# Optimization experiments

Hardware: AMD Instinct MI355X
Metric: run time of the kernel (lower is better)

## Reference

```python
import jax, jax.numpy as jnp
import numpy as np

N_NODES = 50000
N_EDGES = 320000
IN_FEAT = 128
HIDDEN = 256
N_CLASSES = 40
BN_EPS = 1e-5


def _gcn_norm(edge_index, n_nodes):
    # Add self-loops (PyG gcn_norm default) and compute sym-normalized weights
    loops = jnp.arange(n_nodes, dtype=edge_index.dtype)
    src = jnp.concatenate([edge_index[0], loops])
    dst = jnp.concatenate([edge_index[1], loops])
    ones = jnp.ones(src.shape[0], dtype=jnp.float32)
    deg = jax.ops.segment_sum(ones, dst, num_segments=n_nodes)
    dinv = jnp.where(deg > 0, jax.lax.rsqrt(deg), 0.0)
    norm = dinv[src] * dinv[dst]  # [E+N]
    return src, dst, norm


def _gcn_conv(x, src, dst, norm, W, b, n_nodes):
    xw = x @ W                                   # [N, F_out]
    msg = norm[:, None] * xw[src]                # [E+N, F_out] gather
    out = jax.ops.segment_sum(msg, dst, num_segments=n_nodes)  # scatter-add
    return out + b


def _batchnorm(x, gamma, beta):
    mean = jnp.mean(x, axis=0)
    var = jnp.mean(jnp.square(x - mean), axis=0)  # biased, training-mode stats
    return (x - mean) * jax.lax.rsqrt(var + BN_EPS) * gamma + beta


def setup_inputs() -> dict:
    key = jax.random.key(0)
    ks = jax.random.split(key, 8)
    x = jax.random.normal(ks[0], (N_NODES, IN_FEAT), dtype=jnp.float32)
    edge_index = jax.random.randint(ks[1], (2, N_EDGES), 0, N_NODES, dtype=jnp.int64)
    s1 = 1.0 / np.sqrt(IN_FEAT)
    s2 = 1.0 / np.sqrt(HIDDEN)
    return {
        "x": x,
        "edge_index": edge_index,
        "W1": jax.random.normal(ks[2], (IN_FEAT, HIDDEN), dtype=jnp.float32) * s1,
        "b1": jnp.zeros((HIDDEN,), dtype=jnp.float32),
        "g1": jnp.ones((HIDDEN,), dtype=jnp.float32),
        "be1": jnp.zeros((HIDDEN,), dtype=jnp.float32),
        "W2": jax.random.normal(ks[3], (HIDDEN, HIDDEN), dtype=jnp.float32) * s2,
        "b2": jnp.zeros((HIDDEN,), dtype=jnp.float32),
        "g2": jnp.ones((HIDDEN,), dtype=jnp.float32),
        "be2": jnp.zeros((HIDDEN,), dtype=jnp.float32),
        "W3": jax.random.normal(ks[4], (HIDDEN, N_CLASSES), dtype=jnp.float32) * s2,
        "b3": jnp.zeros((N_CLASSES,), dtype=jnp.float32),
    }


def reference(x, edge_index, W1, b1, g1, be1, W2, b2, g2, be2, W3, b3):
    n = x.shape[0]
    src, dst, norm = _gcn_norm(edge_index, n)
    # layer 1
    h = _gcn_conv(x, src, dst, norm, W1, b1, n)
    h = jax.nn.relu(_batchnorm(h, g1, be1))
    # layer 2
    h = _gcn_conv(h, src, dst, norm, W2, b2, n)
    h = jax.nn.relu(_batchnorm(h, g2, be2))
    # output layer
    h = _gcn_conv(h, src, dst, norm, W3, b3, n)
    return jax.nn.log_softmax(h, axis=1)
```

## Files before the change

### kernel.cpp

```cpp
#include <hip/hip_runtime.h>

#define N_NODES 50000
#define N_EDGES 320000
#define IN_FEAT 128
#define HIDDEN  256
#define NCLS    40
#define BN_EPS  1e-5f

#define SCAN_B  256
#define SCAN_NB ((N_NODES + SCAN_B - 1) / SCAN_B)
#define GNB     (N_NODES / 16)

#define PREP_HIST_NB  (N_EDGES / 256)
#define PREP_CVT_NB   (N_NODES * IN_FEAT / 8 / 256)
#define PREP_PACK_NB  54
#define BNA_NB        (N_NODES * HIDDEN / 8 / 256)

typedef __attribute__((ext_vector_type(8))) _Float16 f16x8;
typedef __attribute__((ext_vector_type(2))) _Float16 f16x2;
typedef __attribute__((ext_vector_type(4))) float f32x4;

__device__ __forceinline__ f16x2 pkmax0(f16x2 a) {
    return __builtin_elementwise_max(a, (f16x2)(_Float16)0.f);
}

__device__ __forceinline__ void packB_unit(const float* __restrict__ W,
                                           _Float16* __restrict__ Bp,
                                           int nt, int kt, int nkt, int M, int lane) {
    const int n = nt * 16 + (lane & 15);
    const int kb = kt * 32 + (lane >> 4) * 8;
    _Float16* dst = Bp + (((size_t)nt * nkt + kt) * 64 + lane) * 8;
#pragma unroll
    for (int j = 0; j < 8; j++)
        dst[j] = (n < M) ? (_Float16)W[(size_t)(kb + j) * M + n] : (_Float16)0.f;
}

__global__ __launch_bounds__(256) void k_prep(const int* __restrict__ e_dst,
                                              int* __restrict__ counts,
                                              const float* __restrict__ x,
                                              _Float16* __restrict__ Xh,
                                              const float* __restrict__ W1,
                                              const float* __restrict__ W2,
                                              const float* __restrict__ W3,
                                              _Float16* __restrict__ W1p,
                                              _Float16* __restrict__ W2p,
                                              _Float16* __restrict__ W3p) {
    const int b = blockIdx.x;
    const int tid = threadIdx.x;
    if (b < PREP_HIST_NB) {
        const int e = b * 256 + tid;
        atomicAdd(&counts[e_dst[e]], 1);
    } else if (b < PREP_HIST_NB + PREP_CVT_NB) {
        const int i = (b - PREP_HIST_NB) * 256 + tid;
        float4 a = *(const float4*)(x + (size_t)i * 8);
        float4 c = *(const float4*)(x + (size_t)i * 8 + 4);
        f16x8 o = {(_Float16)a.x, (_Float16)a.y, (_Float16)a.z, (_Float16)a.w,
                   (_Float16)c.x, (_Float16)c.y, (_Float16)c.z, (_Float16)c.w};
        *(f16x8*)&Xh[(size_t)i * 8] = o;
    } else {
        const int wave = tid >> 6, lane = tid & 63;
        const int u = (b - PREP_HIST_NB - PREP_CVT_NB) * 4 + wave;
        if (u < 64) {
            packB_unit(W1, W1p, u >> 2, u & 3, 4, HIDDEN, lane);
        } else if (u < 192) {
            const int v = u - 64;
            packB_unit(W2, W2p, v >> 3, v & 7, 8, HIDDEN, lane);
        } else {
            const int v = u - 192;
            packB_unit(W3, W3p, v >> 3, v & 7, 8, NCLS, lane);
        }
    }
}

__global__ __launch_bounds__(SCAN_B) void k_scan_local(const int* __restrict__ counts,
                                                       int* __restrict__ rowp,
                                                       int* __restrict__ partials) {
    __shared__ int s[SCAN_B];
    const int tid = threadIdx.x;
    const int i = blockIdx.x * SCAN_B + tid;
    int v = (i < N_NODES) ? counts[i] : 0;
    s[tid] = v;
    __syncthreads();
    for (int off = 1; off < SCAN_B; off <<= 1) {
        int t = (tid >= off) ? s[tid - off] : 0;
        __syncthreads();
        s[tid] += t;
        __syncthreads();
    }
    if (i < N_NODES) rowp[i] = s[tid] - v;
    if (tid == SCAN_B - 1) partials[blockIdx.x] = s[SCAN_B - 1];
}

__global__ __launch_bounds__(SCAN_B) void k_scan_add(int* __restrict__ rowp,
                                                     int* __restrict__ cursor,
                                                     const int* __restrict__ partials,
                                                     const int* __restrict__ counts,
                                                     float* __restrict__ dinv) {
    __shared__ int s[SCAN_B];
    const int tid = threadIdx.x;
    const int b = blockIdx.x;
    int v = (tid < b) ? partials[tid] : 0;
    s[tid] = v;
    __syncthreads();
    for (int off = SCAN_B / 2; off > 0; off >>= 1) {
        if (tid < off) s[tid] += s[tid + off];
        __syncthreads();
    }
    const int offset = s[0];
    const int i = b * SCAN_B + tid;
    if (i < N_NODES) {
        int r = rowp[i] + offset;
        rowp[i] = r;
        cursor[i] = r;
        dinv[i] = rsqrtf(1.0f + (float)counts[i]);
    }
    if (b == 0 && tid == 0) rowp[N_NODES] = N_EDGES;
}

__global__ void k_scatter(const int* __restrict__ src, const int* __restrict__ dst,
                          int* __restrict__ cursor, const float* __restrict__ dinv,
                          int2* __restrict__ edat) {
    int e = blockIdx.x * blockDim.x + threadIdx.x;
    if (e < N_EDGES) {
        int d = dst[e], s = src[e];
        int p = atomicAdd(&cursor[d], 1);
        int2 v; v.x = s; v.y = __float_as_int(dinv[s] * dinv[d]);
        edat[p] = v;
    }
}

template <int KIN>
__global__ __launch_bounds__(256, 4) void k_fused(const _Float16* __restrict__ Xin,
                                                  const int* __restrict__ rowp,
                                                  const int2* __restrict__ edat,
                                                  const float* __restrict__ dinv,
                                                  const _Float16* __restrict__ Bp,
                                                  const float* __restrict__ bias,
                                                  _Float16* __restrict__ C,
                                                  float* __restrict__ bnp2) {
    constexpr int nkt = KIN / 32;
    constexpr int LROW = KIN + 8;
    constexpr int RW8 = KIN / 8;
    constexpr int NL = KIN / 128;
    __shared__ __align__(16) _Float16 At[16 * LROW];
    const int wave = threadIdx.x >> 6;
    const int lane = threadIdx.x & 63;
    const int sub  = lane >> 4;
    const int t    = lane & 15;
    const int sb   = lane & 48;
    const int node = blockIdx.x * 16 + wave * 4 + sub;

    const int e0 = rowp[node];
    const int deg = rowp[node + 1] - e0;
    int   pidx = 0;
    float pw   = 0.f;
    if (t < deg) {
        const int2 e = edat[e0 + t];
        pidx = e.x;
        pw = __int_as_float(e.y);
    }
    const float dd = dinv[node];
    const f16x2 sw2 = (f16x2)(_Float16)(dd * dd);

    const f16x8* __restrict__ Xr = (const f16x8*)Xin;
    union U8 { f16x8 v; f16x2 h[4]; };

    U8 a[NL];
#pragma unroll
    for (int q = 0; q < NL; q++) {
        U8 r; r.v = Xr[(size_t)node * RW8 + q * 16 + t];
#pragma unroll
        for (int p = 0; p < 4; p++) a[q].h[p] = sw2 * r.h[p];
    }

    auto batch8 = [&](int j0) {
        int bi[8]; _Float16 bw[8];
#pragma unroll
        for (int j = 0; j < 8; j++) {
            const int   v  = __shfl(pidx, sb + j0 + j);
            const float wv = __shfl(pw,  sb + j0 + j);
            const bool ok = (j0 + j) < deg;
            bi[j] = ok ? v : node;
            bw[j] = ok ? (_Float16)wv : (_Float16)0.f;
        }
        U8 r[8][NL];
#pragma unroll
        for (int j = 0; j < 8; j++)
#pragma unroll
            for (int q = 0; q < NL; q++)
                r[j][q].v = Xr[(size_t)bi[j] * RW8 + q * 16 + t];
        __builtin_amdgcn_sched_barrier(0);
#pragma unroll
        for (int j = 0; j < 8; j++) {
            const f16x2 w2 = (f16x2)bw[j];
#pragma unroll
            for (int q = 0; q < NL; q++)
#pragma unroll
                for (int p = 0; p < 4; p++) a[q].h[p] = w2 * r[j][q].h[p] + a[q].h[p];
        }
    };
    batch8(0);
    if (__any(deg > 8)) {
        batch8(8);
        if (__any(deg > 16)) {
            for (int j = 16; j < deg; j++) {
                const int2 ed = edat[e0 + j];
                const f16x2 w2 = (f16x2)(_Float16)__int_as_float(ed.y);
#pragma unroll
                for (int q = 0; q < NL; q++) {
                    U8 r; r.v = Xr[(size_t)ed.x * RW8 + q * 16 + t];
#pragma unroll
                    for (int p = 0; p < 4; p++) a[q].h[p] = w2 * r.h[p] + a[q].h[p];
                }
            }
        }
    }
#pragma unroll
    for (int q = 0; q < NL; q++)
        *(f16x8*)&At[(wave * 4 + sub) * LROW + q * 128 + t * 8] = a[q].v;
    __syncthreads();

    const int rowb = blockIdx.x * 16;
    const int ntile0 = wave * 4;
    const _Float16* aL = &At[(lane & 15) * LROW + (lane >> 4) * 8];
    f32x4 acc[4] = {};
#pragma unroll
    for (int kt = 0; kt < nkt; kt++) {
        f16x8 af = *(const f16x8*)(aL + kt * 32);
#pragma unroll
        for (int nt = 0; nt < 4; nt++) {
            f16x8 bfr = *(const f16x8*)(Bp + (((size_t)(ntile0 + nt) * nkt + kt) * 64 + lane) * 8);
            acc[nt] = __builtin_amdgcn_mfma_f32_16x16x32_f16(af, bfr, acc[nt], 0, 0, 0);
        }
    }
    const int rg = lane >> 4, cc = lane & 15;
    float s[4], q2[4];
#pragma unroll
    for (int nt = 0; nt < 4; nt++) {
        const int col = (ntile0 + nt) * 16 + cc;
        const float b = bias[col];
        f32x4 a2 = acc[nt];
        a2[0] += b; a2[1] += b; a2[2] += b; a2[3] += b;
        const size_t base = (size_t)(rowb + rg * 4) * HIDDEN + col;
#pragma unroll
        for (int i = 0; i < 4; i++) C[base + (size_t)i * HIDDEN] = (_Float16)a2[i];
        s[nt] = a2[0] + a2[1] + a2[2] + a2[3];
        q2[nt] = a2[0]*a2[0] + a2[1]*a2[1] + a2[2]*a2[2] + a2[3]*a2[3];
    }
#pragma unroll
    for (int nt = 0; nt < 4; nt++) {
        s[nt] += __shfl_xor(s[nt], 16); s[nt] += __shfl_xor(s[nt], 32);
        q2[nt] += __shfl_xor(q2[nt], 16); q2[nt] += __shfl_xor(q2[nt], 32);
    }
    if (lane < 16) {
        float* dst = bnp2 + ((blockIdx.x & 31) * 512) + ntile0 * 16 + lane;
#pragma unroll
        for (int nt = 0; nt < 4; nt++) {
            atomicAdd(&dst[nt * 16], s[nt]);
            atomicAdd(&dst[nt * 16 + 256], q2[nt]);
        }
    }
}

__global__ __launch_bounds__(256) void k_bnprep(const float* __restrict__ bnp2,
                                                const float* __restrict__ g,
                                                const float* __restrict__ be,
                                                float* __restrict__ scale,
                                                float* __restrict__ shift) {
    const int f = threadIdx.x;
    float s = 0.f, q = 0.f;
#pragma unroll
    for (int b = 0; b < 32; b++) {
        s += bnp2[(size_t)b * 512 + f];
        q += bnp2[(size_t)b * 512 + 256 + f];
    }
    const float inv_n = 1.0f / (float)N_NODES;
    float mean = s * inv_n;
    float var = q * inv_n - mean * mean;
    var = fmaxf(var, 0.f);
    float sc = g[f] * rsqrtf(var + BN_EPS);
    scale[f] = sc;
    shift[f] = be[f] - mean * sc;
}

__global__ __launch_bounds__(256) void k_bnapply(_Float16* __restrict__ H,
                                                 const float* __restrict__ scale,
                                                 const float* __restrict__ shift) {
    const size_t i = (size_t)blockIdx.x * 256 + threadIdx.x;
    const int f0 = (int)(i & 31) * 8;
    union U8 { f16x8 v; f16x2 h[4]; } r;
    r.v = ((const f16x8*)H)[i];
#pragma unroll
    for (int p = 0; p < 4; p++) {
        f16x2 sc = {(_Float16)scale[f0 + 2 * p], (_Float16)scale[f0 + 2 * p + 1]};
        f16x2 sh = {(_Float16)shift[f0 + 2 * p], (_Float16)shift[f0 + 2 * p + 1]};
        r.h[p] = pkmax0(sc * r.h[p] + sh);
    }
    ((f16x8*)H)[i] = r.v;
}

template <int K_>
__global__ __launch_bounds__(64) void k_gemm3(const _Float16* __restrict__ A,
                                              const _Float16* __restrict__ Bp,
                                              const float* __restrict__ scale,
                                              const float* __restrict__ shift,
                                              _Float16* __restrict__ C) {
    constexpr int nkt = K_ / 32;
    constexpr int MT = 3;
    const int lane = threadIdx.x & 63;
    const int rowb = blockIdx.x * 16;
    const int koff = (lane >> 4) * 8;
    const _Float16* aptr = A + (size_t)(rowb + (lane & 15)) * K_ + koff;
    f32x4 acc[MT] = {};
#pragma unroll
    for (int kt = 0; kt < nkt; kt++) {
        union { f16x8 v; f16x2 h[4]; } au, tu;
        au.v = *(const f16x8*)(aptr + kt * 32);
        const int kb = kt * 32 + koff;
#pragma unroll
        for (int p = 0; p < 4; p++) {
            f16x2 sc2 = {(_Float16)scale[kb + 2 * p], (_Float16)scale[kb + 2 * p + 1]};
            f16x2 sh2 = {(_Float16)shift[kb + 2 * p], (_Float16)shift[kb + 2 * p + 1]};
            tu.h[p] = pkmax0(sc2 * au.h[p] + sh2);
        }
#pragma unroll
        for (int nt = 0; nt < MT; nt++) {
            f16x8 bfr = *(const f16x8*)(Bp + (((size_t)nt * nkt + kt) * 64 + lane) * 8);
            acc[nt] = __builtin_amdgcn_mfma_f32_16x16x32_f16(tu.v, bfr, acc[nt], 0, 0, 0);
        }
    }
    const int rg = lane >> 4, cc = lane & 15;
#pragma unroll
    for (int nt = 0; nt < MT; nt++) {
        const int col = nt * 16 + cc;
        if (col < NCLS) {
            const size_t base = (size_t)(rowb + rg * 4) * NCLS + col;
#pragma unroll
            for (int i = 0; i < 4; i++) C[base + (size_t)i * NCLS] = (_Float16)acc[nt][i];
        }
    }
}

__global__ __launch_bounds__(256) void k_out(const _Float16* __restrict__ XW,
                                             const int* __restrict__ rowp,
                                             const int2* __restrict__ edat,
                                             const float* __restrict__ dinv,
                                             const float* __restrict__ bias,
                                             float* __restrict__ out) {
    const int wave = threadIdx.x >> 6;
    const int lane = threadIdx.x & 63;
    const int node = blockIdx.x * 4 + wave;
    const float dd = dinv[node];
    const bool act = lane < NCLS;
    const int e0 = rowp[node];
    const int deg = rowp[node + 1] - e0;
    int pidx = 0; float pw = 0.f;
    if (lane < deg) {
        const int2 e = edat[e0 + lane];
        pidx = e.x; pw = __int_as_float(e.y);
    }
    const _Float16* Xl = XW + lane;
    float acc = 0.f;
    if (act) acc = dd * dd * (float)Xl[(size_t)node * NCLS];
    auto batch8 = [&](int j0) {
        int bi[8]; float bw[8];
#pragma unroll
        for (int j = 0; j < 8; j++) {
            const int   v  = __shfl(pidx, j0 + j);
            const float wv = __shfl(pw,  j0 + j);
            const bool ok = (j0 + j) < deg;
            bi[j] = ok ? v : node;
            bw[j] = ok ? wv : 0.f;
        }
        if (act) {
            float rv[8];
#pragma unroll
            for (int j = 0; j < 8; j++) rv[j] = (float)Xl[(size_t)bi[j] * NCLS];
            __builtin_amdgcn_sched_barrier(0);
#pragma unroll
            for (int j = 0; j < 8; j++) acc += bw[j] * rv[j];
        }
    };
    batch8(0);
    if (deg > 8) {
        batch8(8);
        if (deg > 16) {
            batch8(16);
            if (deg > 24) {
                batch8(24);
                if (deg > 32) {
                    for (int j = 32; j < deg; j++) {
                        const int2 ed = edat[e0 + j];
                        if (act) acc += __int_as_float(ed.y) * (float)Xl[(size_t)ed.x * NCLS];
                    }
                }
            }
        }
    }
    if (act) acc += bias[lane];
    float m = act ? acc : -1e30f;
#pragma unroll
    for (int off = 32; off > 0; off >>= 1) m = fmaxf(m, __shfl_xor(m, off));
    float e = act ? expf(acc - m) : 0.f;
#pragma unroll
    for (int off = 32; off > 0; off >>= 1) e += __shfl_xor(e, off);
    const float lse = m + logf(e);
    if (act) out[node * NCLS + lane] = acc - lse;
}

extern "C" void kernel_launch(void* const* d_in, const int* in_sizes, int n_in,
                              void* d_out, int out_size, void* d_ws, size_t ws_size,
                              hipStream_t stream) {
    const float* x   = (const float*)d_in[0];
    const int*   ei  = (const int*)d_in[1];
    const float* W1  = (const float*)d_in[2];
    const float* b1  = (const float*)d_in[3];
    const float* g1  = (const float*)d_in[4];
    const float* be1 = (const float*)d_in[5];
    const float* W2  = (const float*)d_in[6];
    const float* b2  = (const float*)d_in[7];
    const float* g2  = (const float*)d_in[8];
    const float* be2 = (const float*)d_in[9];
    const float* W3  = (const float*)d_in[10];
    const float* b3  = (const float*)d_in[11];
    float* out = (float*)d_out;

    const int* e_src = ei;
    const int* e_dst = ei + N_EDGES;

    char* w = (char*)d_ws;
    _Float16* Xh  = (_Float16*)w;              w += (size_t)N_NODES * IN_FEAT * 2;
    _Float16* H1h = (_Float16*)w;              w += (size_t)N_NODES * HIDDEN * 2;
    _Float16* H2h = (_Float16*)w;              w += (size_t)N_NODES * HIDDEN * 2;
    _Float16* XW3h = (_Float16*)w;             w += (size_t)N_NODES * NCLS * 2;
    float* dinv   = (float*)w;                 w += (size_t)N_NODES * 4;
    int2*  edat   = (int2*)w;                  w += (size_t)N_EDGES * 8;
    int*   counts = (int*)w;                   w += (size_t)N_NODES * 4;
    float* bnp2a  = (float*)w;                 w += (size_t)32 * 512 * 4;
    float* bnp2b  = (float*)w;                 w += (size_t)32 * 512 * 4;
    int*   rowp   = (int*)w;                   w += (size_t)(N_NODES + 4) * 4;
    int*   cursor = (int*)w;                   w += (size_t)N_NODES * 4;
    int*   partials=(int*)w;                   w += 256 * 4;
    float* scale1 = (float*)w;                 w += 256 * 4;
    float* shift1 = (float*)w;                 w += 256 * 4;
    float* scale2 = (float*)w;                 w += 256 * 4;
    float* shift2 = (float*)w;                 w += 256 * 4;
    _Float16* W1p = (_Float16*)w;              w += (size_t)16 * 4 * 64 * 8 * 2;
    _Float16* W2p = (_Float16*)w;              w += (size_t)16 * 8 * 64 * 8 * 2;
    _Float16* W3p = (_Float16*)w;              w += (size_t)3 * 8 * 64 * 8 * 2;

    const int EB = (N_EDGES + 255) / 256;

    hipMemsetAsync(counts, 0, (size_t)N_NODES * 4 + 2 * (size_t)32 * 512 * 4, stream);
    k_prep<<<PREP_HIST_NB + PREP_CVT_NB + PREP_PACK_NB, 256, 0, stream>>>(
        e_dst, counts, x, Xh, W1, W2, W3, W1p, W2p, W3p);
    k_scan_local<<<SCAN_NB, SCAN_B, 0, stream>>>(counts, rowp, partials);
    k_scan_add<<<SCAN_NB, SCAN_B, 0, stream>>>(rowp, cursor, partials, counts, dinv);
    k_scatter<<<EB, 256, 0, stream>>>(e_src, e_dst, cursor, dinv, edat);

    k_fused<IN_FEAT><<<GNB, 256, 0, stream>>>(
        Xh, rowp, edat, dinv, W1p, b1, H1h, bnp2a);
    k_bnprep<<<1, 256, 0, stream>>>(bnp2a, g1, be1, scale1, shift1);
    k_bnapply<<<BNA_NB, 256, 0, stream>>>(H1h, scale1, shift1);

    k_fused<HIDDEN><<<GNB, 256, 0, stream>>>(
        H1h, rowp, edat, dinv, W2p, b2, H2h, bnp2b);
    k_bnprep<<<1, 256, 0, stream>>>(bnp2b, g2, be2, scale2, shift2);

    k_gemm3<HIDDEN><<<GNB, 64, 0, stream>>>(H2h, W3p, scale2, shift2, XW3h);
    k_out<<<N_NODES / 4, 256, 0, stream>>>(XW3h, rowp, edat, dinv, b3, out);
}
```

Before: 243.7 us.

## Split fused aggregate+GEMM into feature-chunked aggregation and separate GEMM kernels

Replaces the fused kernel, which aggregated neighbor rows into LDS and then ran the MFMA GEMM, with two kernels. The first aggregates 32-feature chunks per block, with 4 lanes per node, and writes the result to a new global buffer. The second loads 16-row tiles from that buffer and runs the MFMA GEMM plus bias and BN partial statistics. This aims to raise parallelism and shrink per-thread register footprint in the gather, at the cost of an extra global write and read of the aggregated features and an extra launch per layer.

```diff
diff --git a/kernel.cpp b/kernel.cpp
--- a/kernel.cpp
+++ b/kernel.cpp
@@ -10,6 +10,7 @@
 #define SCAN_B  256
 #define SCAN_NB ((N_NODES + SCAN_B - 1) / SCAN_B)
 #define GNB     (N_NODES / 16)
+#define AGG_T   ((N_NODES + 63) / 64)
 
 #define PREP_HIST_NB  (N_EDGES / 256)
 #define PREP_CVT_NB   (N_NODES * IN_FEAT / 8 / 256)
@@ -130,73 +131,68 @@
 }
 
 template <int KIN>
-__global__ __launch_bounds__(256, 4) void k_fused(const _Float16* __restrict__ Xin,
-                                                  const int* __restrict__ rowp,
-                                                  const int2* __restrict__ edat,
-                                                  const float* __restrict__ dinv,
-                                                  const _Float16* __restrict__ Bp,
-                                                  const float* __restrict__ bias,
-                                                  _Float16* __restrict__ C,
-                                                  float* __restrict__ bnp2) {
-    constexpr int nkt = KIN / 32;
-    constexpr int LROW = KIN + 8;
+__global__ __launch_bounds__(256, 4) void k_agg(const _Float16* __restrict__ Xin,
+                                                const int* __restrict__ rowp,
+                                                const int2* __restrict__ edat,
+                                                const float* __restrict__ dinv,
+                                                _Float16* __restrict__ Hagg) {
+    constexpr int NCH = KIN / 32;
     constexpr int RW8 = KIN / 8;
-    constexpr int NL = KIN / 128;
-    __shared__ __align__(16) _Float16 At[16 * LROW];
+    const int chunk = blockIdx.x % NCH;
+    const int tile  = blockIdx.x / NCH;
+    const int lane = threadIdx.x & 63;
     const int wave = threadIdx.x >> 6;
-    const int lane = threadIdx.x & 63;
-    const int sub  = lane >> 4;
-    const int t    = lane & 15;
-    const int sb   = lane & 48;
-    const int node = blockIdx.x * 16 + wave * 4 + sub;
-
+    const int sub  = lane >> 2;
+    const int t    = lane & 3;
+    const int sb   = lane & 60;
+    int node = tile * 64 + wave * 16 + sub;
+    const bool valid = node < N_NODES;
+    if (!valid) node = N_NODES - 1;
     const int e0 = rowp[node];
-    const int deg = rowp[node + 1] - e0;
-    int   pidx = 0;
-    float pw   = 0.f;
-    if (t < deg) {
-        const int2 e = edat[e0 + t];
-        pidx = e.x;
-        pw = __int_as_float(e.y);
-    }
+    const int deg = valid ? (rowp[node + 1] - e0) : 0;
+
+    int pidx[4]; float pw[4];
+#pragma unroll
+    for (int k = 0; k < 4; k++) {
+        const int j = t + 4 * k;
+        pidx[k] = node; pw[k] = 0.f;
+        if (j < deg) {
+            const int2 e = edat[e0 + j];
+            pidx[k] = e.x; pw[k] = __int_as_float(e.y);
+        }
+    }
+    const int wi = chunk * 4 + t;
     const float dd = dinv[node];
     const f16x2 sw2 = (f16x2)(_Float16)(dd * dd);
-
     const f16x8* __restrict__ Xr = (const f16x8*)Xin;
     union U8 { f16x8 v; f16x2 h[4]; };
 
-    U8 a[NL];
-#pragma unroll
-    for (int q = 0; q < NL; q++) {
-        U8 r; r.v = Xr[(size_t)node * RW8 + q * 16 + t];
-#pragma unroll
-        for (int p = 0; p < 4; p++) a[q].h[p] = sw2 * r.h[p];
-    }
-
+    U8 a;
+    {
+        U8 r; r.v = Xr[(size_t)node * RW8 + wi];
+#pragma unroll
+        for (int p = 0; p < 4; p++) a.h[p] = sw2 * r.h[p];
+    }
     auto batch8 = [&](int j0) {
         int bi[8]; _Float16 bw[8];
 #pragma unroll
         for (int j = 0; j < 8; j++) {
-            const int   v  = __shfl(pidx, sb + j0 + j);
-            const float wv = __shfl(pw,  sb + j0 + j);
-            const bool ok = (j0 + j) < deg;
+            const int jj = j0 + j;
+            const int   v  = __shfl(pidx[jj >> 2], sb + (jj & 3));
+            const float wv = __shfl(pw[jj >> 2],  sb + (jj & 3));
+            const bool ok = jj < deg;
             bi[j] = ok ? v : node;
             bw[j] = ok ? (_Float16)wv : (_Float16)0.f;
         }
-        U8 r[8][NL];
-#pragma unroll
-        for (int j = 0; j < 8; j++)
-#pragma unroll
-            for (int q = 0; q < NL; q++)
-                r[j][q].v = Xr[(size_t)bi[j] * RW8 + q * 16 + t];
+        U8 r[8];
+#pragma unroll
+        for (int j = 0; j < 8; j++) r[j].v = Xr[(size_t)bi[j] * RW8 + wi];
         __builtin_amdgcn_sched_barrier(0);
 #pragma unroll
         for (int j = 0; j < 8; j++) {
             const f16x2 w2 = (f16x2)bw[j];
 #pragma unroll
-            for (int q = 0; q < NL; q++)
-#pragma unroll
-                for (int p = 0; p < 4; p++) a[q].h[p] = w2 * r[j][q].h[p] + a[q].h[p];
+            for (int p = 0; p < 4; p++) a.h[p] = w2 * r[j].h[p] + a.h[p];
         }
     };
     batch8(0);
@@ -206,21 +202,38 @@
             for (int j = 16; j < deg; j++) {
                 const int2 ed = edat[e0 + j];
                 const f16x2 w2 = (f16x2)(_Float16)__int_as_float(ed.y);
-#pragma unroll
-                for (int q = 0; q < NL; q++) {
-                    U8 r; r.v = Xr[(size_t)ed.x * RW8 + q * 16 + t];
-#pragma unroll
-                    for (int p = 0; p < 4; p++) a[q].h[p] = w2 * r.h[p] + a[q].h[p];
-                }
+                U8 r; r.v = Xr[(size_t)ed.x * RW8 + wi];
+#pragma unroll
+                for (int p = 0; p < 4; p++) a.h[p] = w2 * r.h[p] + a.h[p];
             }
         }
     }
-#pragma unroll
-    for (int q = 0; q < NL; q++)
-        *(f16x8*)&At[(wave * 4 + sub) * LROW + q * 128 + t * 8] = a[q].v;
+    if (valid) *(f16x8*)&Hagg[(size_t)node * KIN + wi * 8] = a.v;
+}
+
+template <int KIN>
+__global__ __launch_bounds__(256, 4) void k_gemm(const _Float16* __restrict__ Hagg,
+                                                 const _Float16* __restrict__ Bp,
+                                                 const float* __restrict__ bias,
+                                                 _Float16* __restrict__ C,
+                                                 float* __restrict__ bnp2) {
+    constexpr int nkt = KIN / 32;
+    constexpr int LROW = KIN + 8;
+    constexpr int RW8 = KIN / 8;
+    __shared__ __align__(16) _Float16 At[16 * LROW];
+    const int tid = threadIdx.x;
+    const int rowb = blockIdx.x * 16;
+#pragma unroll
+    for (int it = 0; it < (16 * RW8) / 256; it++) {
+        const int w = it * 256 + tid;
+        const int rr = w / RW8, cw = w % RW8;
+        *(f16x8*)&At[rr * LROW + cw * 8] =
+            ((const f16x8*)Hagg)[(size_t)rowb * RW8 + w];
+    }
     __syncthreads();
 
-    const int rowb = blockIdx.x * 16;
+    const int wave = threadIdx.x >> 6;
+    const int lane = threadIdx.x & 63;
     const int ntile0 = wave * 4;
     const _Float16* aL = &At[(lane & 15) * LROW + (lane >> 4) * 8];
     f32x4 acc[4] = {};
@@ -432,6 +445,7 @@
     _Float16* Xh  = (_Float16*)w;              w += (size_t)N_NODES * IN_FEAT * 2;
     _Float16* H1h = (_Float16*)w;              w += (size_t)N_NODES * HIDDEN * 2;
     _Float16* H2h = (_Float16*)w;              w += (size_t)N_NODES * HIDDEN * 2;
+    _Float16* Sagg = (_Float16*)w;             w += (size_t)N_NODES * HIDDEN * 2;
     _Float16* XW3h = (_Float16*)w;             w += (size_t)N_NODES * NCLS * 2;
     float* dinv   = (float*)w;                 w += (size_t)N_NODES * 4;
     int2*  edat   = (int2*)w;                  w += (size_t)N_EDGES * 8;
@@ -458,13 +472,15 @@
     k_scan_add<<<SCAN_NB, SCAN_B, 0, stream>>>(rowp, cursor, partials, counts, dinv);
     k_scatter<<<EB, 256, 0, stream>>>(e_src, e_dst, cursor, dinv, edat);
 
-    k_fused<IN_FEAT><<<GNB, 256, 0, stream>>>(
-        Xh, rowp, edat, dinv, W1p, b1, H1h, bnp2a);
+    k_agg<IN_FEAT><<<AGG_T * (IN_FEAT / 32), 256, 0, stream>>>(
+        Xh, rowp, edat, dinv, Sagg);
+    k_gemm<IN_FEAT><<<GNB, 256, 0, stream>>>(Sagg, W1p, b1, H1h, bnp2a);
     k_bnprep<<<1, 256, 0, stream>>>(bnp2a, g1, be1, scale1, shift1);
     k_bnapply<<<BNA_NB, 256, 0, stream>>>(H1h, scale1, shift1);
 
-    k_fused<HIDDEN><<<GNB, 256, 0, stream>>>(
-        H1h, rowp, edat, dinv, W2p, b2, H2h, bnp2b);
+    k_agg<HIDDEN><<<AGG_T * (HIDDEN / 32), 256, 0, stream>>>(
+        H1h, rowp, edat, dinv, Sagg);
+    k_gemm<HIDDEN><<<GNB, 256, 0, stream>>>(Sagg, W2p, b2, H2h, bnp2b);
     k_bnprep<<<1, 256, 0, stream>>>(bnp2b, g2, be2, scale2, shift2);
 
     k_gemm3<HIDDEN><<<GNB, 64, 0, stream>>>(H2h, W3p, scale2, shift2, XW3h);
```

New measurement: 282.8 us. +16.0%, slower.
